# Optimization experiments

Measured on AMD Instinct MI355X. Metric: run time of the kernel, lower is better.

Reference implementation:

```python
import jax, jax.numpy as jnp
import numpy as np

NUM_SAMPLE = 80  # hardcoded in the original forward
NUM_ACT = 6
NUM_OPP = 3


def setup_inputs() -> dict:
    key = jax.random.key(0)
    k0, k1, k2 = jax.random.split(key, 3)
    B, D = 4096, 512
    x = jax.random.normal(k0, (B, D), dtype=jnp.float32)
    # orthogonal init with gain 0.01 -> small weights; approximate scale
    W_opp = jax.random.normal(k1, (NUM_OPP, D, NUM_ACT), dtype=jnp.float32) * 0.01
    b_opp = jnp.zeros((NUM_OPP, NUM_ACT), dtype=jnp.float32)
    W = jax.random.normal(k2, (D + NUM_OPP * NUM_ACT, NUM_ACT), dtype=jnp.float32) * 0.01
    b = jnp.zeros((NUM_ACT,), dtype=jnp.float32)
    return {"x": x, "W_opp": W_opp, "b_opp": b_opp, "W": W, "b": b}


def reference(x, W_opp, b_opp, W, b):
    B, D = x.shape
    # --- opponent actors: small linear + softmax, vectorized over the 3 opponents ---
    logits = jnp.einsum('bd,kda->kba', x, W_opp) + b_opp[:, None, :]   # [3,B,6]
    dist = jax.nn.softmax(logits, axis=-1)                              # [3,B,6]
    logp = jax.nn.log_softmax(logits, axis=-1)
    # entropy.mean() per opponent, then sum/3 == mean over opponents
    entropy = (-(dist * logp).sum(-1)).mean(-1).mean()

    # --- vectorized categorical sampling: 80 samples per opponent per batch elem ---
    skey = jax.random.key(42)
    samples = jax.random.categorical(skey, logits[:, None], axis=-1,
                                     shape=(NUM_OPP, NUM_SAMPLE, B))   # [3,S,B] int

    # gather sampled-action probabilities
    probs = jnp.take_along_axis(dist[:, None], samples[..., None], axis=-1)[..., 0]  # [3,S,B]
    probs_bt = jnp.transpose(probs, (0, 2, 1))                          # [3,B,S]
    p1 = probs_bt[0] * probs_bt[1] * probs_bt[2]                        # [B,S]
    p2 = p1 / p1.sum(axis=1, keepdims=True)                             # normalized joint weights

    # actions3[b,s,k] = sampled action of opponent k, sample s, batch b
    acts = jnp.transpose(samples, (2, 1, 0))                            # [B,S,3]
    oh = jax.nn.one_hot(acts, NUM_ACT, dtype=x.dtype).reshape(B, NUM_SAMPLE, NUM_OPP * NUM_ACT)  # [B,S,18]

    xa = jnp.broadcast_to(x[:, None, :], (B, NUM_SAMPLE, D))            # replicate x per sample
    a = jnp.concatenate([xa, oh], axis=2)                               # [B,S,D+18]
    agent_probs = jax.nn.softmax(a @ W + b, axis=-1)                    # [B,S,6]

    actions_probs = jnp.einsum('bs,bsa->ba', p2, agent_probs)           # [B,6]
    return actions_probs, dist, entropy
```

## Files before the change

### kernel.cpp

```cpp
#include <hip/hip_runtime.h>
#include <stdint.h>

#define NUM_ACT 6
#define NUM_OPP 3
#define NUM_SAMPLE 80
#define BATCH 4096
#define DIM 512
#define ACC_STRIDE 98304
#define TROWS 32
#define ENT_IDX 98304

__device__ __forceinline__ uint32_t rotl32(uint32_t x, int d) {
  return (x << d) | (x >> (32 - d));
}

__device__ __forceinline__ void tf_round4(uint32_t& x0, uint32_t& x1,
                                          int r0, int r1, int r2, int r3) {
  x0 += x1; x1 = rotl32(x1, r0); x1 ^= x0;
  x0 += x1; x1 = rotl32(x1, r1); x1 ^= x0;
  x0 += x1; x1 = rotl32(x1, r2); x1 ^= x0;
  x0 += x1; x1 = rotl32(x1, r3); x1 ^= x0;
}

__device__ __forceinline__ void threefry2x32(uint32_t k0, uint32_t k1,
                                             uint32_t& x0, uint32_t& x1) {
  const uint32_t ks2 = k0 ^ k1 ^ 0x1BD11BDAu;
  x0 += k0;  x1 += k1;
  tf_round4(x0, x1, 13, 15, 26, 6);  x0 += k1;  x1 += ks2 + 1u;
  tf_round4(x0, x1, 17, 29, 16, 24); x0 += ks2; x1 += k0  + 2u;
  tf_round4(x0, x1, 13, 15, 26, 6);  x0 += k0;  x1 += k1  + 3u;
  tf_round4(x0, x1, 17, 29, 16, 24); x0 += k1;  x1 += ks2 + 4u;
  tf_round4(x0, x1, 13, 15, 26, 6);  x0 += ks2; x1 += k0  + 5u;
}

__device__ __forceinline__ float jax_uniform(uint32_t flat_idx) {
  uint32_t x0 = 0u, x1 = flat_idx;
  threefry2x32(0u, 42u, x0, x1);
  uint32_t bits = x0 ^ x1;
  return __uint_as_float((bits >> 9) | 0x3f800000u) - 1.0f;
}

__device__ __forceinline__ void dot4(float& a, float4 u, float4 v) {
  a = fmaf(u.x, v.x, a); a = fmaf(u.y, v.y, a);
  a = fmaf(u.z, v.z, a); a = fmaf(u.w, v.w, a);
}

template<int NCH>
__global__ __launch_bounds__(128) void k1_gemm(
    const float* __restrict__ x, const float* __restrict__ Wopp,
    const float* __restrict__ W, float* __restrict__ part) {
  constexpr int WIDTH = 512 / NCH;
  constexpr int XSTR = WIDTH + 4;
  const int tile = blockIdx.x / NCH;
  const int ch = blockIdx.x % NCH;
  const int rowbase = tile * TROWS;
  const int dbase = ch * WIDTH;
  __shared__ float xs[TROWS * XSTR];
  __shared__ float wt[24 * XSTR];
  const int t = threadIdx.x;

  for (int f = t; f < TROWS * (WIDTH / 4); f += 128) {
    int row = f / (WIDTH / 4), c4 = (f % (WIDTH / 4)) << 2;
    float4 v = *(const float4*)(x + (size_t)(rowbase + row) * DIM + dbase + c4);
    *(float4*)(xs + row * XSTR + c4) = v;
  }
  for (int i = t; i < 24 * WIDTH; i += 128) {
    int c = i % 24, dd = i / 24;
    int d = dbase + dd;
    float v = (c < 18) ? Wopp[(c / 6) * (DIM * 6) + d * 6 + (c % 6)]
                       : W[d * 6 + (c - 18)];
    wt[c * XSTR + dd] = v;
  }
  __syncthreads();

  const int rowg = t >> 3, colg = t & 7;
  float acc[2][3] = {{0.f, 0.f, 0.f}, {0.f, 0.f, 0.f}};
  const float* xp = xs + (rowg * 2) * XSTR;
  const float* wp = wt + (colg * 3) * XSTR;
#pragma unroll 4
  for (int dd = 0; dd < WIDTH; dd += 4) {
    float4 x0 = *(const float4*)(xp + dd);
    float4 x1 = *(const float4*)(xp + XSTR + dd);
    float4 w0 = *(const float4*)(wp + dd);
    float4 w1 = *(const float4*)(wp + XSTR + dd);
    float4 w2 = *(const float4*)(wp + 2 * XSTR + dd);
    dot4(acc[0][0], x0, w0); dot4(acc[0][1], x0, w1); dot4(acc[0][2], x0, w2);
    dot4(acc[1][0], x1, w0); dot4(acc[1][1], x1, w1); dot4(acc[1][2], x1, w2);
  }
  const int r0 = rowbase + rowg * 2, c0 = colg * 3;
  float* p = part + (size_t)ch * ACC_STRIDE;
#pragma unroll
  for (int rr = 0; rr < 2; rr++)
#pragma unroll
    for (int cc = 0; cc < 3; cc++)
      p[(r0 + rr) * 24 + c0 + cc] = acc[rr][cc];
}

#define WSTR 144

template<int NCH>
__global__ __launch_bounds__(256) void k3f(
    const float* __restrict__ part, const float* __restrict__ bopp,
    const float* __restrict__ W, const float* __restrict__ bias,
    float* __restrict__ out, float* __restrict__ ws_H) {
  const int w = threadIdx.x >> 6;
  const int l = threadIdx.x & 63;
  const int b = blockIdx.x * 4 + w;
  __shared__ float lds[4][WSTR];
  float* L = lds[w];

  if (l < 54) {
    float2 v = *(const float2*)(W + DIM * NUM_ACT + 2 * l);
    L[2 * l] = v.x; L[2 * l + 1] = v.y;
  }

  float H = 0.f;
  if (l < NUM_OPP) {
    const int k = l;
    float lg[NUM_ACT];
#pragma unroll
    for (int a = 0; a < NUM_ACT; a++) {
      float s = bopp[k * NUM_ACT + a];
#pragma unroll
      for (int g = 0; g < NCH; g++)
        s += part[g * ACC_STRIDE + b * 24 + k * NUM_ACT + a];
      lg[a] = s;
    }
    float m = lg[0];
#pragma unroll
    for (int a = 1; a < NUM_ACT; a++) m = fmaxf(m, lg[a]);
    float e[NUM_ACT], Z = 0.f;
#pragma unroll
    for (int a = 0; a < NUM_ACT; a++) { e[a] = expf(lg[a] - m); Z += e[a]; }
    float logZ = logf(Z);
#pragma unroll
    for (int a = 0; a < NUM_ACT; a++) {
      float pa = e[a] / Z;
      L[112 + k * NUM_ACT + a] = pa;
      H -= pa * ((lg[a] - m) - logZ);
    }
  } else if (l >= 18 && l < 24) {
    const int a = l - 18;
    float s = bias[a];
#pragma unroll
    for (int g = 0; g < NCH; g++)
      s += part[g * ACC_STRIDE + b * 24 + 18 + a];
    L[136 + a] = s;
  }
  H += __shfl_down(H, 1);
  H += __shfl_down(H, 2);

  float d[18];
#pragma unroll
  for (int i = 0; i < 18; i++) d[i] = L[112 + i];

  int   act_a[3];
  float pr_a[3];
#pragma unroll
  for (int k = 0; k < NUM_OPP; k++) {
    float u = jax_uniform((uint32_t)(k * NUM_SAMPLE + l) * BATCH + (uint32_t)b);
    float c = d[k * 6 + 0], pr = d[k * 6 + 0];
    int sel = 0;
#pragma unroll
    for (int a = 1; a < NUM_ACT; a++) {
      bool take = (u >= c);
      sel += take ? 1 : 0;
      pr = take ? d[k * 6 + a] : pr;
      c += d[k * 6 + a];
    }
    act_a[k] = sel; pr_a[k] = pr;
  }
  float prb = 0.f; int actb = 0;
  if (l < 48) {
    const int k = l >> 4, s = 64 + (l & 15);
    float u = jax_uniform((uint32_t)(k * NUM_SAMPLE + s) * BATCH + (uint32_t)b);
    float c = L[112 + k * 6 + 0], pr = c;
    int sel = 0;
#pragma unroll
    for (int a = 1; a < NUM_ACT; a++) {
      float da = L[112 + k * 6 + a];
      bool take = (u >= c);
      sel += take ? 1 : 0;
      pr = take ? da : pr;
      c += da;
    }
    actb = sel; prb = pr;
  }
  const int tm = l & 15;
  float pb0 = __shfl(prb, tm), pb1 = __shfl(prb, tm + 16), pb2 = __shfl(prb, tm + 32);
  int   ab0 = __shfl(actb, tm), ab1 = __shfl(actb, tm + 16), ab2 = __shfl(actb, tm + 32);

  const bool hasb = l < (NUM_SAMPLE - 64);
  float p1a = pr_a[0] * pr_a[1] * pr_a[2];
  float p1b = 0.f;
  if (hasb) p1b = pb0 * pb1 * pb2;
  float tot = p1a + p1b;
#pragma unroll
  for (int m = 32; m > 0; m >>= 1) tot += __shfl_xor(tot, m);

  float xw[NUM_ACT];
#pragma unroll
  for (int a = 0; a < NUM_ACT; a++) xw[a] = L[136 + a];

  float o[NUM_ACT];
#pragma unroll
  for (int a = 0; a < NUM_ACT; a++) o[a] = 0.f;
  {
    int a0 = act_a[0], a1 = act_a[1], a2 = act_a[2];
    float la[NUM_ACT];
#pragma unroll
    for (int a = 0; a < NUM_ACT; a++)
      la[a] = xw[a] + L[a0 * 6 + a] + L[(6 + a1) * 6 + a] + L[(12 + a2) * 6 + a];
    float m = la[0];
#pragma unroll
    for (int a = 1; a < NUM_ACT; a++) m = fmaxf(m, la[a]);
    float e[NUM_ACT], Z = 0.f;
#pragma unroll
    for (int a = 0; a < NUM_ACT; a++) { e[a] = expf(la[a] - m); Z += e[a]; }
    float wz = (p1a / tot) / Z;
#pragma unroll
    for (int a = 0; a < NUM_ACT; a++) o[a] = wz * e[a];
  }
  if (hasb) {
    float la[NUM_ACT];
#pragma unroll
    for (int a = 0; a < NUM_ACT; a++)
      la[a] = xw[a] + L[ab0 * 6 + a] + L[(6 + ab1) * 6 + a] + L[(12 + ab2) * 6 + a];
    float m = la[0];
#pragma unroll
    for (int a = 1; a < NUM_ACT; a++) m = fmaxf(m, la[a]);
    float e[NUM_ACT], Z = 0.f;
#pragma unroll
    for (int a = 0; a < NUM_ACT; a++) { e[a] = expf(la[a] - m); Z += e[a]; }
    float wz = (p1b / tot) / Z;
#pragma unroll
    for (int a = 0; a < NUM_ACT; a++) o[a] += wz * e[a];
  }
#pragma unroll
  for (int m = 32; m > 0; m >>= 1)
#pragma unroll
    for (int a = 0; a < NUM_ACT; a++) o[a] += __shfl_xor(o[a], m);

  if (l == 0) {
#pragma unroll
    for (int a = 0; a < NUM_ACT; a++) out[b * NUM_ACT + a] = o[a];
    ws_H[b] = H;
  }
  if (l < 18) {
    int k = l / 6, a = l - k * 6;
    out[BATCH * NUM_ACT + ((size_t)k * BATCH + b) * NUM_ACT + a] = L[112 + l];
  }
}

__global__ __launch_bounds__(256) void k_ent(const float* __restrict__ ws_H,
                                             float* __restrict__ out) {
  const int t = threadIdx.x;
  const float4* p = (const float4*)ws_H;
  float s = 0.f;
#pragma unroll
  for (int i = 0; i < 4; i++) {
    float4 v = p[t + 256 * i];
    s += v.x + v.y + v.z + v.w;
  }
#pragma unroll
  for (int m = 32; m > 0; m >>= 1) s += __shfl_xor(s, m);
  __shared__ float sw[4];
  if ((t & 63) == 0) sw[t >> 6] = s;
  __syncthreads();
  if (t == 0)
    out[ENT_IDX] = (sw[0] + sw[1] + sw[2] + sw[3]) * (1.0f / 12288.0f);
}

extern "C" void kernel_launch(void* const* d_in, const int* in_sizes, int n_in,
                              void* d_out, int out_size, void* d_ws, size_t ws_size,
                              hipStream_t stream) {
  const float* x    = (const float*)d_in[0];
  const float* Wopp = (const float*)d_in[1];
  const float* bopp = (const float*)d_in[2];
  const float* W    = (const float*)d_in[3];
  const float* bias = (const float*)d_in[4];
  float* out = (float*)d_out;
  float* part = (float*)d_ws;

  size_t need8 = ((size_t)8 * ACC_STRIDE + BATCH) * sizeof(float);
  if (ws_size >= need8) {
    float* ws_H = part + (size_t)8 * ACC_STRIDE;
    k1_gemm<8><<<(BATCH / TROWS) * 8, 128, 0, stream>>>(x, Wopp, W, part);
    k3f<8><<<BATCH / 4, 256, 0, stream>>>(part, bopp, W, bias, out, ws_H);
    k_ent<<<1, 256, 0, stream>>>(ws_H, out);
  } else {
    float* ws_H = part + (size_t)4 * ACC_STRIDE;
    k1_gemm<4><<<(BATCH / TROWS) * 4, 128, 0, stream>>>(x, Wopp, W, part);
    k3f<4><<<BATCH / 4, 256, 0, stream>>>(part, bopp, W, bias, out, ws_H);
    k_ent<<<1, 256, 0, stream>>>(ws_H, out);
  }
}
```

Before: 86.69 us.

## Fuse entropy reduction into main kernel via atomics and enlarge blocks

Removes the separate entropy-reduction kernel launch: k1_gemm zeroes the entropy slot and each k3f block reduces its per-row entropies through shared memory and issues one atomicAdd. k3f blocks grow from 4 to 16 waves (1024 threads), and the partial-sum loads are spread across 24 lanes with shuffles instead of serial per-lane loops. This trades a kernel launch and workspace round trip for a block-wide __syncthreads and atomics, with nondeterministic float summation order.

```diff
diff --git a/kernel.cpp b/kernel.cpp
--- a/kernel.cpp
+++ b/kernel.cpp
@@ -48,7 +48,8 @@
 template<int NCH>
 __global__ __launch_bounds__(128) void k1_gemm(
     const float* __restrict__ x, const float* __restrict__ Wopp,
-    const float* __restrict__ W, float* __restrict__ part) {
+    const float* __restrict__ W, float* __restrict__ part,
+    float* __restrict__ out) {
   constexpr int WIDTH = 512 / NCH;
   constexpr int XSTR = WIDTH + 4;
   const int tile = blockIdx.x / NCH;
@@ -94,19 +95,21 @@
 #pragma unroll
     for (int cc = 0; cc < 3; cc++)
       p[(r0 + rr) * 24 + c0 + cc] = acc[rr][cc];
+  if (blockIdx.x == 0 && t == 0) out[ENT_IDX] = 0.f;
 }
 
 #define WSTR 144
 
 template<int NCH>
-__global__ __launch_bounds__(256) void k3f(
+__global__ __launch_bounds__(1024) void k3f(
     const float* __restrict__ part, const float* __restrict__ bopp,
     const float* __restrict__ W, const float* __restrict__ bias,
-    float* __restrict__ out, float* __restrict__ ws_H) {
+    float* __restrict__ out) {
   const int w = threadIdx.x >> 6;
   const int l = threadIdx.x & 63;
-  const int b = blockIdx.x * 4 + w;
-  __shared__ float lds[4][WSTR];
+  const int b = blockIdx.x * 16 + w;
+  __shared__ float lds[16][WSTR];
+  __shared__ float s_Hw[16];
   float* L = lds[w];
 
   if (l < 54) {
@@ -114,18 +117,24 @@
     L[2 * l] = v.x; L[2 * l + 1] = v.y;
   }
 
+  float colsum = 0.f;
+  if (l < 24) {
+    float s = (l < 18) ? bopp[l] : bias[l - 18];
+#pragma unroll
+    for (int g = 0; g < NCH; g++)
+      s += part[g * ACC_STRIDE + b * 24 + l];
+    colsum = s;
+    if (l >= 18) L[136 + (l - 18)] = s;
+  }
+  const int kk = (l < NUM_OPP) ? l : 0;
+  float lg[NUM_ACT];
+#pragma unroll
+  for (int a = 0; a < NUM_ACT; a++)
+    lg[a] = __shfl(colsum, kk * NUM_ACT + a);
+
   float H = 0.f;
   if (l < NUM_OPP) {
     const int k = l;
-    float lg[NUM_ACT];
-#pragma unroll
-    for (int a = 0; a < NUM_ACT; a++) {
-      float s = bopp[k * NUM_ACT + a];
-#pragma unroll
-      for (int g = 0; g < NCH; g++)
-        s += part[g * ACC_STRIDE + b * 24 + k * NUM_ACT + a];
-      lg[a] = s;
-    }
     float m = lg[0];
 #pragma unroll
     for (int a = 1; a < NUM_ACT; a++) m = fmaxf(m, lg[a]);
@@ -139,16 +148,18 @@
       L[112 + k * NUM_ACT + a] = pa;
       H -= pa * ((lg[a] - m) - logZ);
     }
-  } else if (l >= 18 && l < 24) {
-    const int a = l - 18;
-    float s = bias[a];
-#pragma unroll
-    for (int g = 0; g < NCH; g++)
-      s += part[g * ACC_STRIDE + b * 24 + 18 + a];
-    L[136 + a] = s;
   }
   H += __shfl_down(H, 1);
   H += __shfl_down(H, 2);
+  if (l == 0) s_Hw[w] = H;
+
+  __syncthreads();
+  if (threadIdx.x == 0) {
+    float hs = 0.f;
+#pragma unroll
+    for (int i = 0; i < 16; i++) hs += s_Hw[i];
+    atomicAdd(out + ENT_IDX, hs * (1.0f / 12288.0f));
+  }
 
   float d[18];
 #pragma unroll
@@ -244,31 +255,11 @@
   if (l == 0) {
 #pragma unroll
     for (int a = 0; a < NUM_ACT; a++) out[b * NUM_ACT + a] = o[a];
-    ws_H[b] = H;
   }
   if (l < 18) {
     int k = l / 6, a = l - k * 6;
     out[BATCH * NUM_ACT + ((size_t)k * BATCH + b) * NUM_ACT + a] = L[112 + l];
   }
-}
-
-__global__ __launch_bounds__(256) void k_ent(const float* __restrict__ ws_H,
-                                             float* __restrict__ out) {
-  const int t = threadIdx.x;
-  const float4* p = (const float4*)ws_H;
-  float s = 0.f;
-#pragma unroll
-  for (int i = 0; i < 4; i++) {
-    float4 v = p[t + 256 * i];
-    s += v.x + v.y + v.z + v.w;
-  }
-#pragma unroll
-  for (int m = 32; m > 0; m >>= 1) s += __shfl_xor(s, m);
-  __shared__ float sw[4];
-  if ((t & 63) == 0) sw[t >> 6] = s;
-  __syncthreads();
-  if (t == 0)
-    out[ENT_IDX] = (sw[0] + sw[1] + sw[2] + sw[3]) * (1.0f / 12288.0f);
 }
 
 extern "C" void kernel_launch(void* const* d_in, const int* in_sizes, int n_in,
@@ -282,16 +273,12 @@
   float* out = (float*)d_out;
   float* part = (float*)d_ws;
 
-  size_t need8 = ((size_t)8 * ACC_STRIDE + BATCH) * sizeof(float);
+  size_t need8 = (size_t)8 * ACC_STRIDE * sizeof(float);
   if (ws_size >= need8) {
-    float* ws_H = part + (size_t)8 * ACC_STRIDE;
-    k1_gemm<8><<<(BATCH / TROWS) * 8, 128, 0, stream>>>(x, Wopp, W, part);
-    k3f<8><<<BATCH / 4, 256, 0, stream>>>(part, bopp, W, bias, out, ws_H);
-    k_ent<<<1, 256, 0, stream>>>(ws_H, out);
+    k1_gemm<8><<<(BATCH / TROWS) * 8, 128, 0, stream>>>(x, Wopp, W, part, out);
+    k3f<8><<<BATCH / 16, 1024, 0, stream>>>(part, bopp, W, bias, out);
   } else {
-    float* ws_H = part + (size_t)4 * ACC_STRIDE;
-    k1_gemm<4><<<(BATCH / TROWS) * 4, 128, 0, stream>>>(x, Wopp, W, part);
-    k3f<4><<<BATCH / 4, 256, 0, stream>>>(part, bopp, W, bias, out, ws_H);
-    k_ent<<<1, 256, 0, stream>>>(ws_H, out);
-  }
-}
+    k1_gemm<4><<<(BATCH / TROWS) * 4, 128, 0, stream>>>(x, Wopp, W, part, out);
+    k3f<4><<<BATCH / 16, 1024, 0, stream>>>(part, bopp, W, bias, out);
+  }
+}
```

After: 83.12 us. 4.1% less time.
